# Kernel tuning notes

Hardware: AMD Instinct MI355X
Metric: run time of the kernel (lower is better)

Reference implementation:

```python
import jax, jax.numpy as jnp
import numpy as np


def gcn_conv(x, W, b, src, dst, dinv_sqrt, n_nodes):
    # PyG GCNConv: h = X W; out_i = sum_j norm_ij * h_j + b, norm = d_i^-1/2 d_j^-1/2
    h = x @ W  # [N, out]
    norm = dinv_sqrt[src] * dinv_sqrt[dst]  # [E]
    msg = h[src] * norm[:, None]  # [E, out]
    out = jax.ops.segment_sum(msg, dst, num_segments=n_nodes)
    return out + b


def setup_inputs() -> dict:
    key = jax.random.key(0)
    ks = jax.random.split(key, 12)
    N, E, G = 50000, 400000, 512
    x = jax.random.normal(ks[0], (N, 3), dtype=jnp.float32)
    edge_index = jax.random.randint(ks[1], (2, E), 0, N, dtype=jnp.int64)
    batch = jnp.sort(jax.random.randint(ks[2], (N,), 0, G, dtype=jnp.int64))
    def lin(k, fin, fout):
        kw, kb = jax.random.split(k)
        s = 1.0 / np.sqrt(fin)
        return (jax.random.uniform(kw, (fin, fout), jnp.float32, -s, s),
                jax.random.uniform(kb, (fout,), jnp.float32, -s, s))
    W1, b1 = lin(ks[3], 3, 100)
    W2, b2 = lin(ks[4], 100, 200)
    W3, b3 = lin(ks[5], 200, 100)
    W4, b4 = lin(ks[6], 100, 1)
    return {"x": x, "edge_index": edge_index, "batch": batch, "num_graphs": G,
            "W1": W1, "b1": b1, "W2": W2, "b2": b2,
            "W3": W3, "b3": b3, "W4": W4, "b4": b4}


def reference(x, edge_index, batch, num_graphs, W1, b1, W2, b2, W3, b3, W4, b4):
    N = x.shape[0]
    loop = jnp.arange(N, dtype=edge_index.dtype)
    src = jnp.concatenate([edge_index[0], loop])  # self-loops added (GCNConv default)
    dst = jnp.concatenate([edge_index[1], loop])
    deg = jax.ops.segment_sum(jnp.ones_like(src, dtype=x.dtype), dst, num_segments=N)
    dinv_sqrt = deg ** -0.5  # deg >= 1 due to self-loops

    h = jax.nn.silu(gcn_conv(x, W1, b1, src, dst, dinv_sqrt, N))
    h = jax.nn.silu(gcn_conv(h, W2, b2, src, dst, dinv_sqrt, N))

    # global_mean_pool over `batch` segments
    sums = jax.ops.segment_sum(h, batch, num_segments=num_graphs)  # [G, 200]
    cnts = jax.ops.segment_sum(jnp.ones((N,), h.dtype), batch, num_segments=num_graphs)
    pooled = sums / jnp.maximum(cnts, 1.0)[:, None]

    h = jax.nn.silu(pooled @ W3 + b3)
    out = h @ W4 + b4  # [G, 1]
    return out.squeeze(-1)
```

## Files before the change

### kernel.cpp

```cpp
#include <hip/hip_runtime.h>
#include <math.h>

#define WF 64

__device__ __forceinline__ float silu_f(float v){ return v / (1.0f + expf(-v)); }

typedef __attribute__((ext_vector_type(8))) short bf16x8;
typedef __attribute__((ext_vector_type(4))) float f32x4;

__device__ __forceinline__ void bf16split(float v, unsigned short& h, unsigned short& l){
  unsigned int b = __float_as_uint(v);
  unsigned int hh = (b + 0x8000u) >> 16;
  float hf = __uint_as_float(hh << 16);
  float lo = v - hf;
  unsigned int bl = __float_as_uint(lo);
  h = (unsigned short)hh;
  l = (unsigned short)((bl + 0x8000u) >> 16);
}

__global__ __launch_bounds__(256) void k_count(const int* __restrict__ dst, int* __restrict__ cnt, int E){
  int e = blockIdx.x*blockDim.x + threadIdx.x;
  if (e < E) atomicAdd(&cnt[dst[e]], 1);
}

__global__ __launch_bounds__(256) void k_scan1(const int* __restrict__ cnt, int* __restrict__ rowstart, int* __restrict__ bsum, int N){
  __shared__ int s[256];
  int tid = threadIdx.x;
  int base = blockIdx.x*2048 + tid*8;
  int loc[8]; int tsum = 0;
#pragma unroll
  for (int j=0;j<8;++j){ int idx=base+j; int v = (idx<N)?cnt[idx]:0; loc[j]=tsum; tsum+=v; }
  s[tid]=tsum; __syncthreads();
  for (int off=1; off<256; off<<=1){
    int v = (tid>=off)? s[tid-off] : 0;
    __syncthreads();
    s[tid] += v;
    __syncthreads();
  }
  int texc = s[tid] - tsum;
  if (tid==255) bsum[blockIdx.x] = s[255];
#pragma unroll
  for (int j=0;j<8;++j){ int idx=base+j; if (idx<N) rowstart[idx] = texc + loc[j]; }
}

__global__ __launch_bounds__(256) void k_scan3(const int* __restrict__ bsum, const int* __restrict__ cnt,
                        const float* __restrict__ x,
                        int* __restrict__ rowstart, int* __restrict__ cursor,
                        float* __restrict__ dinv, float4* __restrict__ dxp,
                        int N, int E, int nb){
  __shared__ int boffs;
  int tid = threadIdx.x;
  int b = (blockIdx.x*blockDim.x) >> 11;
  if (tid < WF){
    int v = (tid < nb && tid < b) ? bsum[tid] : 0;
#pragma unroll
    for (int off=32; off; off>>=1) v += __shfl_down(v, off);
    if (tid==0) boffs = v;
  }
  __syncthreads();
  int idx = blockIdx.x*blockDim.x + tid;
  if (idx < N){
    int v = rowstart[idx] + boffs;
    rowstart[idx]=v; cursor[idx]=v;
    float di = rsqrtf((float)(cnt[idx]+1));
    dinv[idx] = di;
    float4 o;
    o.x = di;
    o.y = di*x[3*idx+0];
    o.z = di*x[3*idx+1];
    o.w = di*x[3*idx+2];
    dxp[idx] = o;
  }
  if (idx==0) rowstart[N]=E;
}

__global__ __launch_bounds__(256) void k_fill(const int* __restrict__ src, const int* __restrict__ dst,
                       int* __restrict__ cursor, int* __restrict__ colsrc, int E){
  int e = blockIdx.x*blockDim.x + threadIdx.x;
  if (e < E){
    int d = dst[e];
    int pos = atomicAdd(&cursor[d], 1);
    colsrc[pos] = src[e];
  }
}

__global__ __launch_bounds__(256) void k_wconv(const float* __restrict__ W2,
                       unsigned short* __restrict__ w2th, unsigned short* __restrict__ w2tl){
  int idx = blockIdx.x*blockDim.x + threadIdx.x;
  if (idx < 224*128){
    int f = idx >> 7, k = idx & 127;
    float v = (f < 200 && k < 100) ? W2[(size_t)k*200 + f] : 0.f;
    unsigned short h, l;
    bf16split(v, h, l);
    w2th[idx] = h;
    w2tl[idx] = l;
  }
}

__global__ __launch_bounds__(256) void k_l1(const float4* __restrict__ dxp,
                     const int* __restrict__ rowstart, const int* __restrict__ colsrc,
                     const float* __restrict__ W1, const float* __restrict__ b1,
                     float* __restrict__ h1s, int N){
  __shared__ float w[300];
  __shared__ float bb[100];
  int tid = threadIdx.x;
  for (int t=tid; t<300; t+=blockDim.x) w[t]=W1[t];
  for (int t=tid; t<100; t+=blockDim.x) bb[t]=b1[t];
  __syncthreads();
  int i = blockIdx.x*blockDim.x + tid;
  if (i >= N) return;
  float4 self = dxp[i];
  float di = self.x;
  float sx = self.y, sy = self.z, sz = self.w;
  int jb = rowstart[i], je = rowstart[i+1];
  int j = jb;
  for (; j+3 < je; j += 4){
    float4 r0 = dxp[colsrc[j]];
    float4 r1 = dxp[colsrc[j+1]];
    float4 r2 = dxp[colsrc[j+2]];
    float4 r3 = dxp[colsrc[j+3]];
    sx += (r0.y + r1.y) + (r2.y + r3.y);
    sy += (r0.z + r1.z) + (r2.z + r3.z);
    sz += (r0.w + r1.w) + (r2.w + r3.w);
  }
  for (; j < je; ++j){
    float4 r = dxp[colsrc[j]];
    sx += r.y; sy += r.z; sz += r.w;
  }
  sx*=di; sy*=di; sz*=di;
  float* orow = h1s + (size_t)i*100;
#pragma unroll
  for (int f0=0; f0<100; f0+=4){
    float4 o;
    o.x = silu_f(sx*w[f0+0] + sy*w[100+f0+0] + sz*w[200+f0+0] + bb[f0+0]);
    o.y = silu_f(sx*w[f0+1] + sy*w[100+f0+1] + sz*w[200+f0+1] + bb[f0+1]);
    o.z = silu_f(sx*w[f0+2] + sy*w[100+f0+2] + sz*w[200+f0+2] + bb[f0+2]);
    o.w = silu_f(sx*w[f0+3] + sy*w[100+f0+3] + sz*w[200+f0+3] + bb[f0+3]);
    *(float4*)&orow[f0] = o;
  }
}

__global__ __launch_bounds__(256) void k_agg2(const float* __restrict__ h1s, const int* __restrict__ rowstart,
                       const int* __restrict__ colsrc, const float* __restrict__ dinv,
                       unsigned short* __restrict__ a2h, unsigned short* __restrict__ a2l, int N){
  int node = blockIdx.x*8 + (threadIdx.x >> 5);
  int lane = threadIdx.x & 31;
  if (node >= N) return;
  if (lane >= 25){
    int ko = 100 + (lane-25)*4;
    ushort4 z = make_ushort4(0,0,0,0);
    *(ushort4*)(a2h + (size_t)node*128 + ko) = z;
    *(ushort4*)(a2l + (size_t)node*128 + ko) = z;
    return;
  }
  float di = dinv[node];
  float4 v = *(const float4*)(h1s + (size_t)node*100 + lane*4);
  float4 acc;
  acc.x = di*v.x; acc.y = di*v.y; acc.z = di*v.z; acc.w = di*v.w;
  int jb = rowstart[node], je = rowstart[node+1];
  int j = jb;
  for (; j+1 < je; j += 2){
    int u0 = colsrc[j];   float w0 = dinv[u0];
    int u1 = colsrc[j+1]; float w1 = dinv[u1];
    float4 r0 = *(const float4*)(h1s + (size_t)u0*100 + lane*4);
    float4 r1 = *(const float4*)(h1s + (size_t)u1*100 + lane*4);
    acc.x += w0*r0.x + w1*r1.x;
    acc.y += w0*r0.y + w1*r1.y;
    acc.z += w0*r0.z + w1*r1.z;
    acc.w += w0*r0.w + w1*r1.w;
  }
  if (j < je){
    int u = colsrc[j]; float wv = dinv[u];
    float4 r = *(const float4*)(h1s + (size_t)u*100 + lane*4);
    acc.x += wv*r.x; acc.y += wv*r.y; acc.z += wv*r.z; acc.w += wv*r.w;
  }
  float o[4] = { di*acc.x, di*acc.y, di*acc.z, di*acc.w };
  ushort4 h4, l4;
  bf16split(o[0], h4.x, l4.x);
  bf16split(o[1], h4.y, l4.y);
  bf16split(o[2], h4.z, l4.z);
  bf16split(o[3], h4.w, l4.w);
  *(ushort4*)(a2h + (size_t)node*128 + lane*4) = h4;
  *(ushort4*)(a2l + (size_t)node*128 + lane*4) = l4;
}

__global__ __launch_bounds__(128) void k_mm2(const unsigned short* __restrict__ a2h,
                      const unsigned short* __restrict__ a2l,
                      const unsigned short* __restrict__ w2th,
                      const unsigned short* __restrict__ w2tl,
                      const float* __restrict__ b2, const int* __restrict__ batch,
                      float* __restrict__ pooled, int N){
  __shared__ float plL[256];
  int tid = threadIdx.x;
  int l = tid & 63, w = tid >> 6;
  int n0 = blockIdx.x * 32;
  int row = l & 15;
  int kg  = l >> 4;

  const unsigned short* ah_p = a2h + (size_t)(n0 + w*16 + row)*128;
  const unsigned short* al_p = a2l + (size_t)(n0 + w*16 + row)*128;

  bf16x8 ahf[4], alf[4];
#pragma unroll
  for (int ks = 0; ks < 4; ++ks){
    int ko = ks*32 + kg*8;
    ahf[ks] = *(const bf16x8*)(ah_p + ko);
    alf[ks] = *(const bf16x8*)(al_p + ko);
  }

  int g0 = batch[n0];

  for (int fb = 0; fb < 7; ++fb){
    int gf0 = fb*32 + row, gf1 = gf0 + 16;
    const unsigned short* wh0_p = w2th + (size_t)gf0*128;
    const unsigned short* wl0_p = w2tl + (size_t)gf0*128;
    const unsigned short* wh1_p = w2th + (size_t)gf1*128;
    const unsigned short* wl1_p = w2tl + (size_t)gf1*128;

    f32x4 acc0 = {0.f,0.f,0.f,0.f};
    f32x4 acc1 = {0.f,0.f,0.f,0.f};
#pragma unroll
    for (int ks = 0; ks < 4; ++ks){
      int ko = ks*32 + kg*8;
      bf16x8 wh0 = *(const bf16x8*)(wh0_p + ko);
      bf16x8 wl0 = *(const bf16x8*)(wl0_p + ko);
      bf16x8 wh1 = *(const bf16x8*)(wh1_p + ko);
      bf16x8 wl1 = *(const bf16x8*)(wl1_p + ko);
      acc0 = __builtin_amdgcn_mfma_f32_16x16x32_bf16(ahf[ks], wh0, acc0, 0, 0, 0);
      acc0 = __builtin_amdgcn_mfma_f32_16x16x32_bf16(ahf[ks], wl0, acc0, 0, 0, 0);
      acc0 = __builtin_amdgcn_mfma_f32_16x16x32_bf16(alf[ks], wh0, acc0, 0, 0, 0);
      acc1 = __builtin_amdgcn_mfma_f32_16x16x32_bf16(ahf[ks], wh1, acc1, 0, 0, 0);
      acc1 = __builtin_amdgcn_mfma_f32_16x16x32_bf16(ahf[ks], wl1, acc1, 0, 0, 0);
      acc1 = __builtin_amdgcn_mfma_f32_16x16x32_bf16(alf[ks], wh1, acc1, 0, 0, 0);
    }

    __syncthreads();
    for (int idx = tid; idx < 256; idx += 128) plL[idx] = 0.f;
    __syncthreads();

#pragma unroll
    for (int ft = 0; ft < 2; ++ft){
      f32x4 a = ft ? acc1 : acc0;
      int fl = ft*16 + row;
      int gf = fb*32 + fl;
      if (gf < 200){
        float bias = b2[gf];
        float s = 0.f;
        int gprev = -1;
#pragma unroll
        for (int r = 0; r < 4; ++r){
          int node = n0 + w*16 + kg*4 + r;
          if (node < N){
            int g = batch[node];
            if (g != gprev){
              if (gprev >= 0){
                int dg = gprev - g0;
                if (dg < 8) atomicAdd(&plL[dg*32 + fl], s);
                else        atomicAdd(&pooled[(size_t)gprev*200 + gf], s);
              }
              gprev = g; s = 0.f;
            }
            s += silu_f(a[r] + bias);
          }
        }
        if (gprev >= 0){
          int dg = gprev - g0;
          if (dg < 8) atomicAdd(&plL[dg*32 + fl], s);
          else        atomicAdd(&pooled[(size_t)gprev*200 + gf], s);
        }
      }
    }
    __syncthreads();
    for (int idx = tid; idx < 256; idx += 128){
      float v = plL[idx];
      if (v != 0.f){
        int r = idx >> 5, f = idx & 31;
        int gf = fb*32 + f;
        if (gf < 200) atomicAdd(&pooled[(size_t)(g0+r)*200 + gf], v);
      }
    }
  }
}

__global__ __launch_bounds__(256) void k_head(const float* __restrict__ pooled, const int* __restrict__ batch,
                       const float* __restrict__ W3, const float* __restrict__ b3,
                       const float* __restrict__ W4, const float* __restrict__ b4,
                       float* __restrict__ out, int N){
  __shared__ float pl[200];
  __shared__ float h3[100];
  int g = blockIdx.x; int tid = threadIdx.x;
  int lo=0, hi=N;
  while (lo<hi){ int m=(lo+hi)>>1; if (batch[m] < g) lo=m+1; else hi=m; }
  int s = lo;
  hi=N;
  while (lo<hi){ int m=(lo+hi)>>1; if (batch[m] < g+1) lo=m+1; else hi=m; }
  int e = lo;
  float inv = (e>s) ? 1.0f/(float)(e-s) : 0.0f;
  if (tid < 200) pl[tid] = pooled[(size_t)g*200 + tid] * inv;
  __syncthreads();
  if (tid < 100){
    float acc = b3[tid];
    for (int k=0;k<200;++k) acc += pl[k]*W3[k*100+tid];
    h3[tid] = silu_f(acc);
  }
  __syncthreads();
  if (tid < WF){
    float p = 0.f;
    if (tid < 100)      p  = h3[tid]     * W4[tid];
    if (tid + 64 < 100) p += h3[tid+64]  * W4[tid+64];
#pragma unroll
    for (int off=32; off; off>>=1) p += __shfl_down(p, off);
    if (tid==0) out[g] = p + b4[0];
  }
}

extern "C" void kernel_launch(void* const* d_in, const int* in_sizes, int n_in,
                              void* d_out, int out_size, void* d_ws, size_t ws_size,
                              hipStream_t stream){
  const float* x  = (const float*)d_in[0];
  const int*   ei = (const int*)  d_in[1];
  const int* batch= (const int*)  d_in[2];
  const float* W1 = (const float*)d_in[4];
  const float* b1 = (const float*)d_in[5];
  const float* W2 = (const float*)d_in[6];
  const float* b2 = (const float*)d_in[7];
  const float* W3 = (const float*)d_in[8];
  const float* b3 = (const float*)d_in[9];
  const float* W4 = (const float*)d_in[10];
  const float* b4 = (const float*)d_in[11];
  float* out = (float*)d_out;

  int N = in_sizes[0]/3;
  int E = in_sizes[1]/2;
  int G = out_size;
  const int* src = ei;
  const int* dst = ei + E;
  int NP = ((N + 63)/64)*64;

  char* base = (char*)d_ws; size_t off = 0;
  auto alloc = [&](size_t bytes)->void*{
    void* p = base + off;
    off = (off + bytes + 255) & ~(size_t)255;
    return p;
  };
  int*   cnt      = (int*)  alloc((size_t)N*4);
  float* pooled   = (float*)alloc((size_t)G*200*4);
  size_t zbytes   = off;
  int*   rowstart = (int*)  alloc((size_t)(N+1)*4);
  int*   cursor   = (int*)  alloc((size_t)N*4);
  int*   bsum     = (int*)  alloc(4096);
  int*   colsrc   = (int*)  alloc((size_t)E*4);
  float* dinv     = (float*)alloc((size_t)N*4);
  float4* dxp     = (float4*)alloc((size_t)N*16);
  float* h1s      = (float*)alloc((size_t)N*100*4);
  unsigned short* a2h = (unsigned short*)alloc((size_t)NP*128*2);
  unsigned short* a2l = (unsigned short*)alloc((size_t)NP*128*2);
  unsigned short* w2th = (unsigned short*)alloc((size_t)224*128*2);
  unsigned short* w2tl = (unsigned short*)alloc((size_t)224*128*2);
  (void)ws_size; (void)n_in;

  hipMemsetAsync(base, 0, zbytes, stream);
  int gE = (E+255)/256;
  k_count<<<gE,256,0,stream>>>(dst, cnt, E);
  int nb = (N+2047)/2048;
  k_scan1<<<nb,256,0,stream>>>(cnt, rowstart, bsum, N);
  k_scan3<<<(N+255)/256,256,0,stream>>>(bsum, cnt, x, rowstart, cursor, dinv, dxp, N, E, nb);
  k_wconv<<<(224*128+255)/256,256,0,stream>>>(W2, w2th, w2tl);
  k_fill<<<gE,256,0,stream>>>(src, dst, cursor, colsrc, E);
  k_l1<<<(N+255)/256,256,0,stream>>>(dxp, rowstart, colsrc, W1, b1, h1s, N);
  k_agg2<<<(N+7)/8,256,0,stream>>>(h1s, rowstart, colsrc, dinv, a2h, a2l, N);
  k_mm2<<<(N+31)/32,128,0,stream>>>(a2h, a2l, w2th, w2tl, b2, batch, pooled, N);
  k_head<<<G,256,0,stream>>>(pooled, batch, W3, b3, W4, b4, out, N);
}
```

Before: 189.3 us.

## Restructure k_mm2 pooling into single pass and remap blocks per XCD

k_mm2 now keeps all 14 MFMA accumulator tiles in registers and does the silu/pooling reduction once after the matmul loop. This replaces seven rounds of shared-memory clear, sync, and flush with a single larger 8x224 shared buffer. Block IDs are also remapped so consecutive node tiles land on the same XCD, which should improve L2 locality for the batch and pooled atomics. The cost is higher register pressure from 56 accumulator floats, which may lower occupancy.

```diff
diff --git a/kernel.cpp b/kernel.cpp
--- a/kernel.cpp
+++ b/kernel.cpp
@@ -189,11 +189,15 @@
                       const unsigned short* __restrict__ w2th,
                       const unsigned short* __restrict__ w2tl,
                       const float* __restrict__ b2, const int* __restrict__ batch,
-                      float* __restrict__ pooled, int N){
-  __shared__ float plL[256];
+                      float* __restrict__ pooled, int N, int nwg){
+  __shared__ float plL[8*224];
   int tid = threadIdx.x;
   int l = tid & 63, w = tid >> 6;
-  int n0 = blockIdx.x * 32;
+  int orig = blockIdx.x;
+  int q = nwg >> 3, r = nwg & 7;
+  int xcd = orig % 8, rk = orig / 8;
+  int bid = (xcd < r) ? (xcd*(q+1) + rk) : (r*(q+1) + (xcd-r)*q + rk);
+  int n0 = bid * 32;
   int row = l & 15;
   int kg  = l >> 4;
 
@@ -208,17 +212,18 @@
     alf[ks] = *(const bf16x8*)(al_p + ko);
   }
 
-  int g0 = batch[n0];
-
+  f32x4 accs[14];
+#pragma unroll
+  for (int i=0;i<14;++i) accs[i] = (f32x4){0.f,0.f,0.f,0.f};
+
+#pragma unroll
   for (int fb = 0; fb < 7; ++fb){
     int gf0 = fb*32 + row, gf1 = gf0 + 16;
     const unsigned short* wh0_p = w2th + (size_t)gf0*128;
     const unsigned short* wl0_p = w2tl + (size_t)gf0*128;
     const unsigned short* wh1_p = w2th + (size_t)gf1*128;
     const unsigned short* wl1_p = w2tl + (size_t)gf1*128;
-
-    f32x4 acc0 = {0.f,0.f,0.f,0.f};
-    f32x4 acc1 = {0.f,0.f,0.f,0.f};
+    f32x4 a0 = accs[2*fb], a1 = accs[2*fb+1];
 #pragma unroll
     for (int ks = 0; ks < 4; ++ks){
       int ko = ks*32 + kg*8;
@@ -226,58 +231,57 @@
       bf16x8 wl0 = *(const bf16x8*)(wl0_p + ko);
       bf16x8 wh1 = *(const bf16x8*)(wh1_p + ko);
       bf16x8 wl1 = *(const bf16x8*)(wl1_p + ko);
-      acc0 = __builtin_amdgcn_mfma_f32_16x16x32_bf16(ahf[ks], wh0, acc0, 0, 0, 0);
-      acc0 = __builtin_amdgcn_mfma_f32_16x16x32_bf16(ahf[ks], wl0, acc0, 0, 0, 0);
-      acc0 = __builtin_amdgcn_mfma_f32_16x16x32_bf16(alf[ks], wh0, acc0, 0, 0, 0);
-      acc1 = __builtin_amdgcn_mfma_f32_16x16x32_bf16(ahf[ks], wh1, acc1, 0, 0, 0);
-      acc1 = __builtin_amdgcn_mfma_f32_16x16x32_bf16(ahf[ks], wl1, acc1, 0, 0, 0);
-      acc1 = __builtin_amdgcn_mfma_f32_16x16x32_bf16(alf[ks], wh1, acc1, 0, 0, 0);
+      a0 = __builtin_amdgcn_mfma_f32_16x16x32_bf16(ahf[ks], wh0, a0, 0, 0, 0);
+      a0 = __builtin_amdgcn_mfma_f32_16x16x32_bf16(ahf[ks], wl0, a0, 0, 0, 0);
+      a0 = __builtin_amdgcn_mfma_f32_16x16x32_bf16(alf[ks], wh0, a0, 0, 0, 0);
+      a1 = __builtin_amdgcn_mfma_f32_16x16x32_bf16(ahf[ks], wh1, a1, 0, 0, 0);
+      a1 = __builtin_amdgcn_mfma_f32_16x16x32_bf16(ahf[ks], wl1, a1, 0, 0, 0);
+      a1 = __builtin_amdgcn_mfma_f32_16x16x32_bf16(alf[ks], wh1, a1, 0, 0, 0);
     }
-
-    __syncthreads();
-    for (int idx = tid; idx < 256; idx += 128) plL[idx] = 0.f;
-    __syncthreads();
-
-#pragma unroll
-    for (int ft = 0; ft < 2; ++ft){
-      f32x4 a = ft ? acc1 : acc0;
-      int fl = ft*16 + row;
-      int gf = fb*32 + fl;
-      if (gf < 200){
-        float bias = b2[gf];
-        float s = 0.f;
-        int gprev = -1;
-#pragma unroll
-        for (int r = 0; r < 4; ++r){
-          int node = n0 + w*16 + kg*4 + r;
-          if (node < N){
-            int g = batch[node];
-            if (g != gprev){
-              if (gprev >= 0){
-                int dg = gprev - g0;
-                if (dg < 8) atomicAdd(&plL[dg*32 + fl], s);
-                else        atomicAdd(&pooled[(size_t)gprev*200 + gf], s);
-              }
-              gprev = g; s = 0.f;
+    accs[2*fb] = a0; accs[2*fb+1] = a1;
+  }
+
+  for (int idx = tid; idx < 8*224; idx += 128) plL[idx] = 0.f;
+  __syncthreads();
+
+  int g0 = batch[n0];
+#pragma unroll
+  for (int ft = 0; ft < 14; ++ft){
+    f32x4 a = accs[ft];
+    int gf = (ft >> 1)*32 + (ft & 1)*16 + row;
+    if (gf < 200){
+      float bias = b2[gf];
+      float s = 0.f;
+      int gprev = -1;
+#pragma unroll
+      for (int r2 = 0; r2 < 4; ++r2){
+        int node = n0 + w*16 + kg*4 + r2;
+        if (node < N){
+          int g = batch[node];
+          if (g != gprev){
+            if (gprev >= 0){
+              int dg = gprev - g0;
+              if (dg < 8) atomicAdd(&plL[dg*224 + gf], s);
+              else        atomicAdd(&pooled[(size_t)gprev*200 + gf], s);
             }
-            s += silu_f(a[r] + bias);
+            gprev = g; s = 0.f;
           }
-        }
-        if (gprev >= 0){
-          int dg = gprev - g0;
-          if (dg < 8) atomicAdd(&plL[dg*32 + fl], s);
-          else        atomicAdd(&pooled[(size_t)gprev*200 + gf], s);
+          s += silu_f(a[r2] + bias);
         }
       }
+      if (gprev >= 0){
+        int dg = gprev - g0;
+        if (dg < 8) atomicAdd(&plL[dg*224 + gf], s);
+        else        atomicAdd(&pooled[(size_t)gprev*200 + gf], s);
+      }
     }
-    __syncthreads();
-    for (int idx = tid; idx < 256; idx += 128){
-      float v = plL[idx];
-      if (v != 0.f){
-        int r = idx >> 5, f = idx & 31;
-        int gf = fb*32 + f;
-        if (gf < 200) atomicAdd(&pooled[(size_t)(g0+r)*200 + gf], v);
-      }
+  }
+  __syncthreads();
+  for (int idx = tid; idx < 8*224; idx += 128){
+    float v = plL[idx];
+    if (v != 0.f){
+      int r2 = idx / 224, f = idx - r2*224;
+      if (f < 200) atomicAdd(&pooled[(size_t)(g0+r2)*200 + f], v);
     }
   }
 }
@@ -369,6 +373,7 @@
   k_fill<<<gE,256,0,stream>>>(src, dst, cursor, colsrc, E);
   k_l1<<<(N+255)/256,256,0,stream>>>(dxp, rowstart, colsrc, W1, b1, h1s, N);
   k_agg2<<<(N+7)/8,256,0,stream>>>(h1s, rowstart, colsrc, dinv, a2h, a2l, N);
-  k_mm2<<<(N+31)/32,128,0,stream>>>(a2h, a2l, w2th, w2tl, b2, batch, pooled, N);
+  int nwg = (N+31)/32;
+  k_mm2<<<nwg,128,0,stream>>>(a2h, a2l, w2th, w2tl, b2, batch, pooled, N, nwg);
   k_head<<<G,256,0,stream>>>(pooled, batch, W3, b3, W4, b4, out, N);
 }
```

Result: faster. 184.8 us (-2.4%).

## Recompute layer-1 features on the fly in aggregation and remap mm2 blocks per XCD

Applied to the files above, without the earlier changes.

Layer 1 now stores only a per-node float4 (dinv plus the aggregated 3-d input). The layer-2 aggregation recomputes silu(z W1 + b1) for every neighbor inside the gather loop, so the 100-wide h1 matrix (20 MB) is never written or re-read, and each edge gathers 16 bytes instead of 400. This trades memory traffic for extra ALU work (about 400 FMAs plus 100 exps per edge). Separately, k_mm2 remaps block IDs so that each XCD processes a contiguous range of nodes, which is meant to improve L2 locality for the batch-pooling atomics.

```diff
diff --git a/kernel.cpp b/kernel.cpp
--- a/kernel.cpp
+++ b/kernel.cpp
@@ -46,7 +46,7 @@
 __global__ __launch_bounds__(256) void k_scan3(const int* __restrict__ bsum, const int* __restrict__ cnt,
                         const float* __restrict__ x,
                         int* __restrict__ rowstart, int* __restrict__ cursor,
-                        float* __restrict__ dinv, float4* __restrict__ dxp,
+                        float4* __restrict__ dxp,
                         int N, int E, int nb){
   __shared__ int boffs;
   int tid = threadIdx.x;
@@ -63,7 +63,6 @@
     int v = rowstart[idx] + boffs;
     rowstart[idx]=v; cursor[idx]=v;
     float di = rsqrtf((float)(cnt[idx]+1));
-    dinv[idx] = di;
     float4 o;
     o.x = di;
     o.y = di*x[3*idx+0];
@@ -97,17 +96,10 @@
   }
 }
 
-__global__ __launch_bounds__(256) void k_l1(const float4* __restrict__ dxp,
+__global__ __launch_bounds__(256) void k_z1(const float4* __restrict__ dxp,
                      const int* __restrict__ rowstart, const int* __restrict__ colsrc,
-                     const float* __restrict__ W1, const float* __restrict__ b1,
-                     float* __restrict__ h1s, int N){
-  __shared__ float w[300];
-  __shared__ float bb[100];
-  int tid = threadIdx.x;
-  for (int t=tid; t<300; t+=blockDim.x) w[t]=W1[t];
-  for (int t=tid; t<100; t+=blockDim.x) bb[t]=b1[t];
-  __syncthreads();
-  int i = blockIdx.x*blockDim.x + tid;
+                     float4* __restrict__ z1, int N){
+  int i = blockIdx.x*blockDim.x + threadIdx.x;
   if (i >= N) return;
   float4 self = dxp[i];
   float di = self.x;
@@ -127,24 +119,25 @@
     float4 r = dxp[colsrc[j]];
     sx += r.y; sy += r.z; sz += r.w;
   }
-  sx*=di; sy*=di; sz*=di;
-  float* orow = h1s + (size_t)i*100;
-#pragma unroll
-  for (int f0=0; f0<100; f0+=4){
-    float4 o;
-    o.x = silu_f(sx*w[f0+0] + sy*w[100+f0+0] + sz*w[200+f0+0] + bb[f0+0]);
-    o.y = silu_f(sx*w[f0+1] + sy*w[100+f0+1] + sz*w[200+f0+1] + bb[f0+1]);
-    o.z = silu_f(sx*w[f0+2] + sy*w[100+f0+2] + sz*w[200+f0+2] + bb[f0+2]);
-    o.w = silu_f(sx*w[f0+3] + sy*w[100+f0+3] + sz*w[200+f0+3] + bb[f0+3]);
-    *(float4*)&orow[f0] = o;
-  }
-}
-
-__global__ __launch_bounds__(256) void k_agg2(const float* __restrict__ h1s, const int* __restrict__ rowstart,
-                       const int* __restrict__ colsrc, const float* __restrict__ dinv,
+  float4 o;
+  o.x = di;
+  o.y = di*sx; o.z = di*sy; o.w = di*sz;
+  z1[i] = o;
+}
+
+__global__ __launch_bounds__(256) void k_agg2f(const float4* __restrict__ z1,
+                       const int* __restrict__ rowstart, const int* __restrict__ colsrc,
+                       const float* __restrict__ W1, const float* __restrict__ b1,
                        unsigned short* __restrict__ a2h, unsigned short* __restrict__ a2l, int N){
-  int node = blockIdx.x*8 + (threadIdx.x >> 5);
-  int lane = threadIdx.x & 31;
+  __shared__ float w[300];
+  __shared__ float bb[100];
+  int tid = threadIdx.x;
+  for (int t=tid; t<300; t+=256) w[t]=W1[t];
+  for (int t=tid; t<100; t+=256) bb[t]=b1[t];
+  __syncthreads();
+
+  int node = blockIdx.x*8 + (tid >> 5);
+  int lane = tid & 31;
   if (node >= N) return;
   if (lane >= 25){
     int ko = 100 + (lane-25)*4;
@@ -153,35 +146,48 @@
     *(ushort4*)(a2l + (size_t)node*128 + ko) = z;
     return;
   }
-  float di = dinv[node];
-  float4 v = *(const float4*)(h1s + (size_t)node*100 + lane*4);
-  float4 acc;
-  acc.x = di*v.x; acc.y = di*v.y; acc.z = di*v.z; acc.w = di*v.w;
+  int f0 = lane*4;
+  float w0[4], w1[4], w2[4], b[4];
+#pragma unroll
+  for (int j=0;j<4;++j){
+    w0[j] = w[f0+j]; w1[j] = w[100+f0+j]; w2[j] = w[200+f0+j]; b[j] = bb[f0+j];
+  }
+
+  float4 zn = z1[node];
+  float din = zn.x;
+  float acc[4];
+#pragma unroll
+  for (int j=0;j<4;++j){
+    float h = silu_f(zn.y*w0[j] + zn.z*w1[j] + zn.w*w2[j] + b[j]);
+    acc[j] = din*h;
+  }
   int jb = rowstart[node], je = rowstart[node+1];
-  int j = jb;
-  for (; j+1 < je; j += 2){
-    int u0 = colsrc[j];   float w0 = dinv[u0];
-    int u1 = colsrc[j+1]; float w1 = dinv[u1];
-    float4 r0 = *(const float4*)(h1s + (size_t)u0*100 + lane*4);
-    float4 r1 = *(const float4*)(h1s + (size_t)u1*100 + lane*4);
-    acc.x += w0*r0.x + w1*r1.x;
-    acc.y += w0*r0.y + w1*r1.y;
-    acc.z += w0*r0.z + w1*r1.z;
-    acc.w += w0*r0.w + w1*r1.w;
-  }
-  if (j < je){
-    int u = colsrc[j]; float wv = dinv[u];
-    float4 r = *(const float4*)(h1s + (size_t)u*100 + lane*4);
-    acc.x += wv*r.x; acc.y += wv*r.y; acc.z += wv*r.z; acc.w += wv*r.w;
-  }
-  float o[4] = { di*acc.x, di*acc.y, di*acc.z, di*acc.w };
+  int e = jb;
+  for (; e+1 < je; e += 2){
+    float4 zu0 = z1[colsrc[e]];
+    float4 zu1 = z1[colsrc[e+1]];
+#pragma unroll
+    for (int j=0;j<4;++j){
+      float h0 = silu_f(zu0.y*w0[j] + zu0.z*w1[j] + zu0.w*w2[j] + b[j]);
+      float h1v = silu_f(zu1.y*w0[j] + zu1.z*w1[j] + zu1.w*w2[j] + b[j]);
+      acc[j] += zu0.x*h0 + zu1.x*h1v;
+    }
+  }
+  if (e < je){
+    float4 zu = z1[colsrc[e]];
+#pragma unroll
+    for (int j=0;j<4;++j){
+      float h = silu_f(zu.y*w0[j] + zu.z*w1[j] + zu.w*w2[j] + b[j]);
+      acc[j] += zu.x*h;
+    }
+  }
   ushort4 h4, l4;
-  bf16split(o[0], h4.x, l4.x);
-  bf16split(o[1], h4.y, l4.y);
-  bf16split(o[2], h4.z, l4.z);
-  bf16split(o[3], h4.w, l4.w);
-  *(ushort4*)(a2h + (size_t)node*128 + lane*4) = h4;
-  *(ushort4*)(a2l + (size_t)node*128 + lane*4) = l4;
+  bf16split(din*acc[0], h4.x, l4.x);
+  bf16split(din*acc[1], h4.y, l4.y);
+  bf16split(din*acc[2], h4.z, l4.z);
+  bf16split(din*acc[3], h4.w, l4.w);
+  *(ushort4*)(a2h + (size_t)node*128 + f0) = h4;
+  *(ushort4*)(a2l + (size_t)node*128 + f0) = l4;
 }
 
 __global__ __launch_bounds__(128) void k_mm2(const unsigned short* __restrict__ a2h,
@@ -189,11 +195,15 @@
                       const unsigned short* __restrict__ w2th,
                       const unsigned short* __restrict__ w2tl,
                       const float* __restrict__ b2, const int* __restrict__ batch,
-                      float* __restrict__ pooled, int N){
+                      float* __restrict__ pooled, int N, int nwg){
   __shared__ float plL[256];
   int tid = threadIdx.x;
   int l = tid & 63, w = tid >> 6;
-  int n0 = blockIdx.x * 32;
+  int orig = blockIdx.x;
+  int q = nwg >> 3, r = nwg & 7;
+  int xcd = orig % 8, rk = orig / 8;
+  int bid = (xcd < r) ? (xcd*(q+1) + rk) : (r*(q+1) + (xcd-r)*q + rk);
+  int n0 = bid * 32;
   int row = l & 15;
   int kg  = l >> 4;
 
@@ -248,8 +258,8 @@
         float s = 0.f;
         int gprev = -1;
 #pragma unroll
-        for (int r = 0; r < 4; ++r){
-          int node = n0 + w*16 + kg*4 + r;
+        for (int r2 = 0; r2 < 4; ++r2){
+          int node = n0 + w*16 + kg*4 + r2;
           if (node < N){
             int g = batch[node];
             if (g != gprev){
@@ -260,7 +270,7 @@
               }
               gprev = g; s = 0.f;
             }
-            s += silu_f(a[r] + bias);
+            s += silu_f(a[r2] + bias);
           }
         }
         if (gprev >= 0){
@@ -274,9 +284,9 @@
     for (int idx = tid; idx < 256; idx += 128){
       float v = plL[idx];
       if (v != 0.f){
-        int r = idx >> 5, f = idx & 31;
+        int r2 = idx >> 5, f = idx & 31;
         int gf = fb*32 + f;
-        if (gf < 200) atomicAdd(&pooled[(size_t)(g0+r)*200 + gf], v);
+        if (gf < 200) atomicAdd(&pooled[(size_t)(g0+r2)*200 + gf], v);
       }
     }
   }
@@ -350,9 +360,8 @@
   int*   cursor   = (int*)  alloc((size_t)N*4);
   int*   bsum     = (int*)  alloc(4096);
   int*   colsrc   = (int*)  alloc((size_t)E*4);
-  float* dinv     = (float*)alloc((size_t)N*4);
   float4* dxp     = (float4*)alloc((size_t)N*16);
-  float* h1s      = (float*)alloc((size_t)N*100*4);
+  float4* z1      = (float4*)alloc((size_t)N*16);
   unsigned short* a2h = (unsigned short*)alloc((size_t)NP*128*2);
   unsigned short* a2l = (unsigned short*)alloc((size_t)NP*128*2);
   unsigned short* w2th = (unsigned short*)alloc((size_t)224*128*2);
@@ -364,11 +373,12 @@
   k_count<<<gE,256,0,stream>>>(dst, cnt, E);
   int nb = (N+2047)/2048;
   k_scan1<<<nb,256,0,stream>>>(cnt, rowstart, bsum, N);
-  k_scan3<<<(N+255)/256,256,0,stream>>>(bsum, cnt, x, rowstart, cursor, dinv, dxp, N, E, nb);
+  k_scan3<<<(N+255)/256,256,0,stream>>>(bsum, cnt, x, rowstart, cursor, dxp, N, E, nb);
   k_wconv<<<(224*128+255)/256,256,0,stream>>>(W2, w2th, w2tl);
   k_fill<<<gE,256,0,stream>>>(src, dst, cursor, colsrc, E);
-  k_l1<<<(N+255)/256,256,0,stream>>>(dxp, rowstart, colsrc, W1, b1, h1s, N);
-  k_agg2<<<(N+7)/8,256,0,stream>>>(h1s, rowstart, colsrc, dinv, a2h, a2l, N);
-  k_mm2<<<(N+31)/32,128,0,stream>>>(a2h, a2l, w2th, w2tl, b2, batch, pooled, N);
+  k_z1<<<(N+255)/256,256,0,stream>>>(dxp, rowstart, colsrc, z1, N);
+  k_agg2f<<<(N+7)/8,256,0,stream>>>(z1, rowstart, colsrc, W1, b1, a2h, a2l, N);
+  int nwg = (N+31)/32;
+  k_mm2<<<nwg,128,0,stream>>>(a2h, a2l, w2th, w2tl, b2, batch, pooled, N, nwg);
   k_head<<<G,256,0,stream>>>(pooled, batch, W3, b3, W4, b4, out, N);
 }
```

Result: slower. 217.6 us (+15.0%).
